# Optimization experiments

Measured on AMD Instinct MI355X. Metric: run time of the kernel, lower is better.

The kernel has to match this reference:

```python
import jax, jax.numpy as jnp
import numpy as np
import math

N_EMBD = 1024
D_STATE = 16
D_CONV = 4
EXPAND = 2
D_INNER = EXPAND * N_EMBD          # 2048
DT_RANK = math.ceil(N_EMBD / 16)   # 64
B, L = 2, 2048
LN_EPS = 1e-5


def setup_inputs() -> dict:
    key = jax.random.key(0)
    ks = jax.random.split(key, 12)
    s = lambda fan_in: 1.0 / np.sqrt(fan_in)
    x = jax.random.normal(ks[0], (B, L, N_EMBD), dtype=jnp.float32)
    ln_g = jnp.ones((N_EMBD,), jnp.float32)
    ln_b = jnp.zeros((N_EMBD,), jnp.float32)
    in_proj_w = jax.random.normal(ks[1], (2 * D_INNER, N_EMBD), jnp.float32) * s(N_EMBD)
    conv_w = jax.random.normal(ks[2], (D_INNER, 1, D_CONV), jnp.float32) * s(D_CONV)
    conv_b = jax.random.normal(ks[3], (D_INNER,), jnp.float32) * s(D_CONV)
    x_proj_w = jax.random.normal(ks[4], (DT_RANK + 2 * D_STATE, D_INNER), jnp.float32) * s(D_INNER)
    dt_proj_w = jax.random.normal(ks[5], (D_INNER, DT_RANK), jnp.float32) * s(DT_RANK)
    # dt bias initialized so softplus(dt) is in a reasonable range
    dt = jnp.exp(jax.random.uniform(ks[6], (D_INNER,)) * (np.log(0.1) - np.log(1e-3)) + np.log(1e-3))
    dt_proj_b = dt + jnp.log(-jnp.expm1(-dt))  # inverse softplus
    A_log = jnp.log(jnp.tile(jnp.arange(1, D_STATE + 1, dtype=jnp.float32)[None, :], (D_INNER, 1)))
    D = jnp.ones((D_INNER,), jnp.float32)
    out_proj_w = jax.random.normal(ks[7], (N_EMBD, D_INNER), jnp.float32) * s(D_INNER)
    return {"x": x, "ln_g": ln_g, "ln_b": ln_b, "in_proj_w": in_proj_w,
            "conv_w": conv_w, "conv_b": conv_b, "x_proj_w": x_proj_w,
            "dt_proj_w": dt_proj_w, "dt_proj_b": dt_proj_b,
            "A_log": A_log, "D": D, "out_proj_w": out_proj_w}


def _selective_scan(u, delta, A, Bt, Ct, D):
    # u, delta: (B, L, d_inner); A: (d_inner, d_state); Bt, Ct: (B, L, d_state)
    def step(h, inp):
        d_t, B_t, C_t, u_t = inp          # (B,di) (B,ds) (B,ds) (B,di)
        dA = jnp.exp(d_t[..., None] * A)                     # (B, di, ds)
        dBu = d_t[..., None] * B_t[:, None, :] * u_t[..., None]
        h = dA * h + dBu
        y = jnp.einsum('bds,bs->bd', h, C_t)
        return h, y
    h0 = jnp.zeros((u.shape[0], A.shape[0], A.shape[1]), u.dtype)
    xs = (jnp.swapaxes(delta, 0, 1), jnp.swapaxes(Bt, 0, 1),
          jnp.swapaxes(Ct, 0, 1), jnp.swapaxes(u, 0, 1))
    _, ys = jax.lax.scan(step, h0, xs)    # (L, B, di)
    return jnp.swapaxes(ys, 0, 1) + u * D


def reference(x, ln_g, ln_b, in_proj_w, conv_w, conv_b, x_proj_w,
              dt_proj_w, dt_proj_b, A_log, D, out_proj_w):
    # Pre-LayerNorm
    mu = jnp.mean(x, axis=-1, keepdims=True)
    var = jnp.var(x, axis=-1, keepdims=True)
    x_norm = (x - mu) * jax.lax.rsqrt(var + LN_EPS) * ln_g + ln_b

    # Input projection -> (u, res)
    xz = jnp.einsum('bld,ed->ble', x_norm, in_proj_w)        # (B, L, 2*di)
    u, res = jnp.split(xz, 2, axis=-1)

    # Causal depthwise conv1d over time
    u_c = jnp.swapaxes(u, 1, 2)                              # (B, di, L)
    u_c = jax.lax.conv_general_dilated(
        u_c, conv_w, window_strides=(1,), padding=[(D_CONV - 1, 0)],
        dimension_numbers=('NCH', 'OIH', 'NCH'), feature_group_count=D_INNER)
    u_c = jax.nn.silu(jnp.swapaxes(u_c, 1, 2) + conv_b)      # (B, L, di)

    # SSM parameterization
    x_dbl = jnp.einsum('bld,ed->ble', u_c, x_proj_w)         # (B, L, dt_rank + 2*ds)
    dt, Bt, Ct = jnp.split(x_dbl, [DT_RANK, DT_RANK + D_STATE], axis=-1)
    delta = jax.nn.softplus(jnp.einsum('blr,dr->bld', dt, dt_proj_w) + dt_proj_b)
    A = -jnp.exp(A_log)                                      # (di, ds)

    y = _selective_scan(u_c, delta, A, Bt, Ct, D)            # (B, L, di)
    y = y * jax.nn.silu(res)
    out = jnp.einsum('bld,ed->ble', y, out_proj_w)           # (B, L, n_embd)
    return x + out
```

## Files before the change

### kernel.cpp

```cpp
#include <hip/hip_runtime.h>
#include <hip/hip_bf16.h>
#include <math.h>

#define NE    1024
#define DI    2048
#define LSEQ  2048
#define NB    2
#define DS    16
#define DTR   64
#define XDW   96

#define CCH   64
#define TCH   (LSEQ/CCH)

#define SKX   8
#define XPROJ_PART (4096*96)

typedef __attribute__((ext_vector_type(8))) short short8;
typedef __attribute__((ext_vector_type(4))) float floatx4;

__device__ __forceinline__ float softplus_fast(float x) {
    return (x > 20.f) ? x : __logf(1.f + __expf(x));
}
__device__ __forceinline__ float siluf(float x) {
    return x / (1.f + __expf(-x));
}

__device__ __forceinline__ void gld16(const void* g, void* l) {
    __builtin_amdgcn_global_load_lds(
        (const __attribute__((address_space(1))) unsigned int*)g,
        (__attribute__((address_space(3))) unsigned int*)l, 16, 0, 0);
}

#define F2BF_N1 (4096*1024/4)
#define F2BF_N2 (2048*1024/4)
#define F2BF_N3 (96*2048/4)
#define F2BF_N4 (2048*64/4)
#define LN_BLOCKS 4096
#define F2BF_BLOCKS ((F2BF_N1 + F2BF_N2 + F2BF_N3 + F2BF_N4) / 256)

__global__ __launch_bounds__(256) void prep_kernel(
    const float* __restrict__ x, const float* __restrict__ g,
    const float* __restrict__ b, __hip_bfloat16* __restrict__ xn,
    const float* __restrict__ s1, ushort4* __restrict__ d1,
    const float* __restrict__ s2, ushort4* __restrict__ d2,
    const float* __restrict__ s3, ushort4* __restrict__ d3,
    const float* __restrict__ s4, ushort4* __restrict__ d4)
{
    int tid = threadIdx.x;
    if (blockIdx.x >= LN_BLOCKS) {
        int i = (blockIdx.x - LN_BLOCKS) * 256 + tid;
        const float* src; ushort4* dst; int j;
        if (i < F2BF_N1)                           { src = s1; dst = d1; j = i; }
        else if (i < F2BF_N1 + F2BF_N2)            { src = s2; dst = d2; j = i - F2BF_N1; }
        else if (i < F2BF_N1 + F2BF_N2 + F2BF_N3)  { src = s3; dst = d3; j = i - F2BF_N1 - F2BF_N2; }
        else                                       { src = s4; dst = d4; j = i - F2BF_N1 - F2BF_N2 - F2BF_N3; }
        float4 v = ((const float4*)src)[j];
        union { __hip_bfloat16 h[4]; ushort4 u; } cv;
        cv.h[0] = __float2bfloat16(v.x);
        cv.h[1] = __float2bfloat16(v.y);
        cv.h[2] = __float2bfloat16(v.z);
        cv.h[3] = __float2bfloat16(v.w);
        dst[j] = cv.u;
        return;
    }
    int row = blockIdx.x;
    const float4* xr = (const float4*)(x + (size_t)row * NE);
    float4 v = xr[tid];
    float s  = v.x + v.y + v.z + v.w;
    float sq = v.x*v.x + v.y*v.y + v.z*v.z + v.w*v.w;
    #pragma unroll
    for (int off = 32; off > 0; off >>= 1) {
        s  += __shfl_down(s, off);
        sq += __shfl_down(sq, off);
    }
    __shared__ float ss[4], ssq[4];
    __shared__ float smu, srstd;
    int wv = tid >> 6, lane = tid & 63;
    if (lane == 0) { ss[wv] = s; ssq[wv] = sq; }
    __syncthreads();
    if (tid == 0) {
        float a = ss[0] + ss[1] + ss[2] + ss[3];
        float q = ssq[0] + ssq[1] + ssq[2] + ssq[3];
        float mu  = a * (1.f / NE);
        float var = q * (1.f / NE) - mu * mu;
        smu = mu; srstd = rsqrtf(var + 1e-5f);
    }
    __syncthreads();
    float mu = smu, rstd = srstd;
    float4 gv = ((const float4*)g)[tid];
    float4 bv = ((const float4*)b)[tid];
    union { __hip_bfloat16 h[4]; ushort4 u; } cv;
    cv.h[0] = __float2bfloat16((v.x - mu) * rstd * gv.x + bv.x);
    cv.h[1] = __float2bfloat16((v.y - mu) * rstd * gv.y + bv.y);
    cv.h[2] = __float2bfloat16((v.z - mu) * rstd * gv.z + bv.z);
    cv.h[3] = __float2bfloat16((v.w - mu) * rstd * gv.w + bv.w);
    ((ushort4*)xn)[row * 256 + tid] = cv.u;
}

__global__ __launch_bounds__(256, 2) void gemm_bf16_in(
    const __hip_bfloat16* __restrict__ A,
    const __hip_bfloat16* __restrict__ W,
    __hip_bfloat16* __restrict__ C, int N, int K)
{
    __shared__ __hip_bfloat16 As[128 * 64];
    __shared__ __hip_bfloat16 Bs[256 * 64];
    int tid = threadIdx.x;
    int lane = tid & 63;
    int w = tid >> 6, wr = w >> 1, wc = w & 1;
    int row0 = blockIdx.y * 128, col0 = blockIdx.x * 256;

    int sr = tid >> 3, sc = tid & 7;
    int gc = sc ^ (sr & 7);
    const __hip_bfloat16* ag = A + (size_t)(row0 + sr) * K + gc * 8;
    const __hip_bfloat16* bg = W + (size_t)(col0 + sr) * K + gc * 8;
    char* la_st = (char*)As + w * 1024;
    char* lb_st = (char*)Bs + w * 1024;
    const size_t rs32 = (size_t)32 * K;

    floatx4 acc[4][8];
    #pragma unroll
    for (int i = 0; i < 4; ++i)
        #pragma unroll
        for (int j = 0; j < 8; ++j) acc[i][j] = (floatx4){0.f, 0.f, 0.f, 0.f};

    int m = lane & 15, kq = lane >> 4;
    int s0 = kq ^ (m & 7);
    int s1 = (4 + kq) ^ (m & 7);
    const char* la0 = (const char*)As + (wr * 64 + m) * 128 + s0 * 16;
    const char* la1 = (const char*)As + (wr * 64 + m) * 128 + s1 * 16;
    const char* lb0 = (const char*)Bs + (wc * 128 + m) * 128 + s0 * 16;
    const char* lb1 = (const char*)Bs + (wc * 128 + m) * 128 + s1 * 16;

    for (int k0 = 0; k0 < K; k0 += 64) {
        #pragma unroll
        for (int j = 0; j < 4; ++j)
            gld16(ag + j * rs32, la_st + j * 4096);
        #pragma unroll
        for (int j = 0; j < 8; ++j)
            gld16(bg + j * rs32, lb_st + j * 4096);
        ag += 64; bg += 64;
        __syncthreads();
        {
            short8 af[4], bf[8];
            #pragma unroll
            for (int i = 0; i < 4; ++i) af[i] = *(const short8*)(la0 + i * 2048);
            #pragma unroll
            for (int j = 0; j < 8; ++j) bf[j] = *(const short8*)(lb0 + j * 2048);
            #pragma unroll
            for (int i = 0; i < 4; ++i)
                #pragma unroll
                for (int j = 0; j < 8; ++j)
                    acc[i][j] = __builtin_amdgcn_mfma_f32_16x16x32_bf16(
                        af[i], bf[j], acc[i][j], 0, 0, 0);
        }
        {
            short8 af[4], bf[8];
            #pragma unroll
            for (int i = 0; i < 4; ++i) af[i] = *(const short8*)(la1 + i * 2048);
            #pragma unroll
            for (int j = 0; j < 8; ++j) bf[j] = *(const short8*)(lb1 + j * 2048);
            #pragma unroll
            for (int i = 0; i < 4; ++i)
                #pragma unroll
                for (int j = 0; j < 8; ++j)
                    acc[i][j] = __builtin_amdgcn_mfma_f32_16x16x32_bf16(
                        af[i], bf[j], acc[i][j], 0, 0, 0);
        }
        __syncthreads();
    }

    int crow = row0 + wr * 64 + kq * 4;
    int ccol = col0 + wc * 128 + m;
    #pragma unroll
    for (int i = 0; i < 4; ++i)
        #pragma unroll
        for (int j = 0; j < 8; ++j)
            #pragma unroll
            for (int r2 = 0; r2 < 4; ++r2) {
                size_t rr = (size_t)(crow + i * 16 + r2);
                int cc = ccol + j * 16;
                C[rr * N + cc] = __float2bfloat16(acc[i][j][r2]);
            }
}

__global__ __launch_bounds__(256) void dtproj_mfma(
    const __hip_bfloat16* __restrict__ A,
    const __hip_bfloat16* __restrict__ W,
    const float* __restrict__ bias,
    __hip_bfloat16* __restrict__ dlt)
{
    __shared__ __hip_bfloat16 As[128 * 64];
    __shared__ __hip_bfloat16 Bs[128 * 64];
    int tid = threadIdx.x;
    int lane = tid & 63;
    int w = tid >> 6, wr = w >> 1, wc = w & 1;
    int row0 = blockIdx.y * 128, col0 = blockIdx.x * 128;
    const int K = DTR;

    int sr = tid >> 3, sc = tid & 7;
    int gc = sc ^ (sr & 7);
    const __hip_bfloat16* ag = A + (size_t)(row0 + sr) * K + gc * 8;
    const __hip_bfloat16* bg = W + (size_t)(col0 + sr) * K + gc * 8;
    char* la_st = (char*)As + w * 1024;
    char* lb_st = (char*)Bs + w * 1024;
    const size_t rs32 = (size_t)32 * K;

    #pragma unroll
    for (int j = 0; j < 4; ++j) {
        gld16(ag + j * rs32, la_st + j * 4096);
        gld16(bg + j * rs32, lb_st + j * 4096);
    }

    floatx4 acc[4][4];
    #pragma unroll
    for (int i = 0; i < 4; ++i)
        #pragma unroll
        for (int j = 0; j < 4; ++j) acc[i][j] = (floatx4){0.f, 0.f, 0.f, 0.f};

    int m = lane & 15, kq = lane >> 4;
    int s0 = kq ^ (m & 7);
    int s1 = (4 + kq) ^ (m & 7);
    const char* la0 = (const char*)As + (wr * 64 + m) * 128 + s0 * 16;
    const char* la1 = (const char*)As + (wr * 64 + m) * 128 + s1 * 16;
    const char* lb0 = (const char*)Bs + (wc * 64 + m) * 128 + s0 * 16;
    const char* lb1 = (const char*)Bs + (wc * 64 + m) * 128 + s1 * 16;
    __syncthreads();
    {
        short8 af[4], bf[4];
        #pragma unroll
        for (int i = 0; i < 4; ++i) {
            af[i] = *(const short8*)(la0 + i * 2048);
            bf[i] = *(const short8*)(lb0 + i * 2048);
        }
        #pragma unroll
        for (int i = 0; i < 4; ++i)
            #pragma unroll
            for (int j = 0; j < 4; ++j)
                acc[i][j] = __builtin_amdgcn_mfma_f32_16x16x32_bf16(
                    af[i], bf[j], acc[i][j], 0, 0, 0);
    }
    {
        short8 af[4], bf[4];
        #pragma unroll
        for (int i = 0; i < 4; ++i) {
            af[i] = *(const short8*)(la1 + i * 2048);
            bf[i] = *(const short8*)(lb1 + i * 2048);
        }
        #pragma unroll
        for (int i = 0; i < 4; ++i)
            #pragma unroll
            for (int j = 0; j < 4; ++j)
                acc[i][j] = __builtin_amdgcn_mfma_f32_16x16x32_bf16(
                    af[i], bf[j], acc[i][j], 0, 0, 0);
    }

    int crow = row0 + wr * 64 + kq * 4;
    int ccol = col0 + wc * 64 + m;
    float bj[4];
    #pragma unroll
    for (int j = 0; j < 4; ++j) bj[j] = bias[ccol + j * 16];
    #pragma unroll
    for (int i = 0; i < 4; ++i)
        #pragma unroll
        for (int j = 0; j < 4; ++j)
            #pragma unroll
            for (int r2 = 0; r2 < 4; ++r2) {
                size_t rr = (size_t)(crow + i * 16 + r2);
                int cc = ccol + j * 16;
                dlt[rr * DI + cc] =
                    __float2bfloat16(softplus_fast(acc[i][j][r2] + bj[j]));
            }
}

__global__ __launch_bounds__(256) void gemm_bf16_n128(
    const __hip_bfloat16* __restrict__ A,
    const __hip_bfloat16* __restrict__ W,
    const float* __restrict__ resid,
    float* __restrict__ C, int N, int K)
{
    __shared__ __hip_bfloat16 As[64 * 64];
    __shared__ __hip_bfloat16 Bs[128 * 64];
    int tid = threadIdx.x;
    int lane = tid & 63;
    int w = tid >> 6;
    int row0 = blockIdx.y * 64, col0 = blockIdx.x * 128;

    int sr = tid >> 3, sc = tid & 7;
    int gc = sc ^ (sr & 7);
    const __hip_bfloat16* ag = A + (size_t)(row0 + sr) * K + gc * 8;
    const __hip_bfloat16* bg = W + (size_t)(col0 + sr) * K + gc * 8;
    char* la_st = (char*)As + w * 1024;
    char* lb_st = (char*)Bs + w * 1024;
    const size_t rs32 = (size_t)32 * K;

    floatx4 acc[4][2];
    #pragma unroll
    for (int i = 0; i < 4; ++i)
        #pragma unroll
        for (int j = 0; j < 2; ++j) acc[i][j] = (floatx4){0.f, 0.f, 0.f, 0.f};

    int m = lane & 15, kq = lane >> 4;
    int s0 = kq ^ (m & 7);
    int s1 = (4 + kq) ^ (m & 7);
    const char* la0 = (const char*)As + m * 128 + s0 * 16;
    const char* la1 = (const char*)As + m * 128 + s1 * 16;
    const char* lb0 = (const char*)Bs + (w * 32 + m) * 128 + s0 * 16;
    const char* lb1 = (const char*)Bs + (w * 32 + m) * 128 + s1 * 16;

    for (int k0 = 0; k0 < K; k0 += 64) {
        gld16(ag,        la_st);
        gld16(ag + rs32, la_st + 4096);
        #pragma unroll
        for (int j = 0; j < 4; ++j)
            gld16(bg + j * rs32, lb_st + j * 4096);
        ag += 64; bg += 64;
        __syncthreads();
        {
            short8 af[4], bf[2];
            #pragma unroll
            for (int i = 0; i < 4; ++i) af[i] = *(const short8*)(la0 + i * 2048);
            #pragma unroll
            for (int j = 0; j < 2; ++j) bf[j] = *(const short8*)(lb0 + j * 2048);
            #pragma unroll
            for (int i = 0; i < 4; ++i)
                #pragma unroll
                for (int j = 0; j < 2; ++j)
                    acc[i][j] = __builtin_amdgcn_mfma_f32_16x16x32_bf16(
                        af[i], bf[j], acc[i][j], 0, 0, 0);
        }
        {
            short8 af[4], bf[2];
            #pragma unroll
            for (int i = 0; i < 4; ++i) af[i] = *(const short8*)(la1 + i * 2048);
            #pragma unroll
            for (int j = 0; j < 2; ++j) bf[j] = *(const short8*)(lb1 + j * 2048);
            #pragma unroll
            for (int i = 0; i < 4; ++i)
                #pragma unroll
                for (int j = 0; j < 2; ++j)
                    acc[i][j] = __builtin_amdgcn_mfma_f32_16x16x32_bf16(
                        af[i], bf[j], acc[i][j], 0, 0, 0);
        }
        __syncthreads();
    }

    int crow = row0 + kq * 4;
    int ccol = col0 + w * 32 + m;
    #pragma unroll
    for (int i = 0; i < 4; ++i)
        #pragma unroll
        for (int j = 0; j < 2; ++j)
            #pragma unroll
            for (int r2 = 0; r2 < 4; ++r2) {
                size_t rr = (size_t)(crow + i * 16 + r2);
                int cc = ccol + j * 16;
                C[rr * N + cc] = acc[i][j][r2] + resid[rr * N + cc];
            }
}

__global__ __launch_bounds__(256) void xproj_kernel(
    const __hip_bfloat16* __restrict__ A,
    const __hip_bfloat16* __restrict__ W,
    float* __restrict__ xpart)
{
    int tid = threadIdx.x;
    int lane = tid & 63;
    int w = tid >> 6;
    int kz = blockIdx.y;
    int row0 = blockIdx.x * 128 + w * 32;
    int m  = lane & 15;
    int kq = lane >> 4;

    floatx4 acc[2][6];
    #pragma unroll
    for (int i = 0; i < 2; ++i)
        #pragma unroll
        for (int j = 0; j < 6; ++j) acc[i][j] = (floatx4){0.f, 0.f, 0.f, 0.f};

    const __hip_bfloat16* a0 = A + (size_t)(row0 + m) * DI + kz * (DI / SKX) + kq * 8;
    const __hip_bfloat16* b0 = W + (size_t)m * DI + kz * (DI / SKX) + kq * 8;

    #pragma unroll
    for (int ks = 0; ks < (DI / SKX) / 32; ++ks) {
        short8 af0 = *(const short8*)(a0);
        short8 af1 = *(const short8*)(a0 + (size_t)16 * DI);
        #pragma unroll
        for (int j = 0; j < 6; ++j) {
            short8 bf = *(const short8*)(b0 + (size_t)j * 16 * DI);
            acc[0][j] = __builtin_amdgcn_mfma_f32_16x16x32_bf16(af0, bf, acc[0][j], 0, 0, 0);
            acc[1][j] = __builtin_amdgcn_mfma_f32_16x16x32_bf16(af1, bf, acc[1][j], 0, 0, 0);
        }
        a0 += 32; b0 += 32;
    }

    float* cp = xpart + (size_t)kz * XPROJ_PART;
    int crow = row0 + kq * 4;
    #pragma unroll
    for (int i = 0; i < 2; ++i)
        #pragma unroll
        for (int j = 0; j < 6; ++j)
            #pragma unroll
            for (int r = 0; r < 4; ++r)
                cp[(size_t)(crow + i * 16 + r) * XDW + j * 16 + m] = acc[i][j][r];
}

__global__ __launch_bounds__(256) void reduce8_kernel(
    const float* __restrict__ part, float* __restrict__ xdbl,
    __hip_bfloat16* __restrict__ dtx)
{
    int i = blockIdx.x * 256 + threadIdx.x;
    float s = 0.f;
    #pragma unroll
    for (int k = 0; k < SKX; ++k) s += part[(size_t)k * XPROJ_PART + i];
    xdbl[i] = s;
    int row = i / XDW;
    int col = i - row * XDW;
    if (col < DTR)
        dtx[(size_t)row * DTR + col] = __float2bfloat16(s);
}

__global__ __launch_bounds__(256) void conv_silu_kernel(
    const __hip_bfloat16* __restrict__ xz, const float* __restrict__ cw,
    const float* __restrict__ cb, ushort4* __restrict__ uc_bf)
{
    int i4 = blockIdx.x * 256 + threadIdx.x;
    int d4 = i4 & 511;
    int bt = i4 >> 9;
    int t  = bt & (LSEQ - 1);
    int d  = d4 * 4;
    float4 w0 = *(const float4*)(cw + (size_t)(d+0) * 4);
    float4 w1 = *(const float4*)(cw + (size_t)(d+1) * 4);
    float4 w2 = *(const float4*)(cw + (size_t)(d+2) * 4);
    float4 w3 = *(const float4*)(cw + (size_t)(d+3) * 4);
    const float* wt0 = (const float*)&w0;
    const float* wt1 = (const float*)&w1;
    const float* wt2 = (const float*)&w2;
    const float* wt3 = (const float*)&w3;
    float4 acc = *(const float4*)(cb + d);
    const __hip_bfloat16* base = xz + ((size_t)bt << 12) + d;
    #pragma unroll
    for (int k = 0; k < 4; ++k) {
        int tp = t - 3 + k;
        if (tp >= 0) {
            union { ushort4 u; __hip_bfloat16 h[4]; } raw;
            raw.u = *(const ushort4*)(base - ((size_t)(3 - k) << 12));
            acc.x = fmaf(wt0[k], __bfloat162float(raw.h[0]), acc.x);
            acc.y = fmaf(wt1[k], __bfloat162float(raw.h[1]), acc.y);
            acc.z = fmaf(wt2[k], __bfloat162float(raw.h[2]), acc.z);
            acc.w = fmaf(wt3[k], __bfloat162float(raw.h[3]), acc.w);
        }
    }
    union { __hip_bfloat16 h[4]; ushort4 u; } cv;
    cv.h[0] = __float2bfloat16(siluf(acc.x));
    cv.h[1] = __float2bfloat16(siluf(acc.y));
    cv.h[2] = __float2bfloat16(siluf(acc.z));
    cv.h[3] = __float2bfloat16(siluf(acc.w));
    uc_bf[i4] = cv.u;
}

template<bool FINAL>
__global__ __launch_bounds__(256) void scan_chunk_kernel(
    const __hip_bfloat16* __restrict__ dlt, const __hip_bfloat16* __restrict__ uc,
    const float* __restrict__ xdbl, const float* __restrict__ A_log,
    const float* __restrict__ Dp, const __hip_bfloat16* __restrict__ xz,
    float* __restrict__ P, float* __restrict__ S,
    __hip_bfloat16* __restrict__ y)
{
    __shared__ float sBC[TCH][32];
    int tid = threadIdx.x;
    int d = blockIdx.x * 256 + tid;
    int c = blockIdx.y;
    int b = blockIdx.z;
    int row0 = b * LSEQ + c * TCH;

    {
        int tt = tid >> 3, j4 = (tid & 7) * 4;
        const float4* src = (const float4*)(xdbl + (size_t)(row0 + tt) * XDW + DTR + j4);
        *(float4*)(&sBC[tt][j4]) = *src;
    }
    __syncthreads();

    float Ac[DS], h[DS], p[DS];
    #pragma unroll
    for (int s = 0; s < DS; ++s) {
        Ac[s] = -expf(A_log[(size_t)d * DS + s]);
        p[s] = 1.f;
    }
    float Ac0 = Ac[0];
    bool fast = true;
    #pragma unroll
    for (int s = 1; s < DS; ++s)
        fast = fast && (fabsf(Ac[s] - (float)(s + 1) * Ac0) <= 1e-3f * fabsf(Ac[s]));

    size_t soff = (((size_t)b * CCH + c) * DI + d) * DS;
    if (FINAL) {
        #pragma unroll
        for (int s = 0; s < DS; ++s) h[s] = S[soff + s];
    } else {
        #pragma unroll
        for (int s = 0; s < DS; ++s) h[s] = 0.f;
    }
    float Dd = Dp[d];
    size_t ix = (size_t)row0 * DI + d;

    if (fast) {
        float p1 = 1.f;
        float dv = __bfloat162float(dlt[ix]);
        float ut = __bfloat162float(uc[ix]);
        for (int tt = 0; tt < TCH; ++tt) {
            float dv_n = 0.f, ut_n = 0.f;
            if (tt + 1 < TCH) {
                dv_n = __bfloat162float(dlt[ix + DI]);
                ut_n = __bfloat162float(uc[ix + DI]);
            }
            float du = dv * ut;
            float e1 = __expf(dv * Ac0);
            float e = 1.f;
            float yacc = 0.f;
            #pragma unroll
            for (int s = 0; s < DS; ++s) {
                e *= e1;
                h[s] = fmaf(e, h[s], du * sBC[tt][s]);
                if (FINAL) yacc = fmaf(h[s], sBC[tt][16 + s], yacc);
            }
            if (!FINAL) p1 *= e1;
            if (FINAL) {
                float res = __bfloat162float(xz[((size_t)(row0 + tt) << 12) + DI + d]);
                y[ix] = __float2bfloat16(fmaf(ut, Dd, yacc) * siluf(res));
            }
            ix += DI;
            dv = dv_n; ut = ut_n;
        }
        if (!FINAL) {
            float e = 1.f;
            #pragma unroll
            for (int s = 0; s < DS; ++s) { e *= p1; p[s] = e; }
        }
    } else {
        for (int tt = 0; tt < TCH; ++tt) {
            float dv = __bfloat162float(dlt[ix]);
            float ut = __bfloat162float(uc[ix]);
            float du = dv * ut;
            float yacc = 0.f;
            #pragma unroll
            for (int s = 0; s < DS; ++s) {
                float e = __expf(dv * Ac[s]);
                h[s] = fmaf(e, h[s], du * sBC[tt][s]);
                if (FINAL) yacc = fmaf(h[s], sBC[tt][16 + s], yacc);
                else       p[s] *= e;
            }
            if (FINAL) {
                float res = __bfloat162float(xz[((size_t)(row0 + tt) << 12) + DI + d]);
                y[ix] = __float2bfloat16(fmaf(ut, Dd, yacc) * siluf(res));
            }
            ix += DI;
        }
    }
    if (!FINAL) {
        #pragma unroll
        for (int s = 0; s < DS; ++s) { P[soff + s] = p[s]; S[soff + s] = h[s]; }
    }
}

__global__ __launch_bounds__(256) void scan_combine_kernel(
    const float* __restrict__ P, float* __restrict__ S)
{
    int idx = blockIdx.x * 256 + threadIdx.x;
    int b = idx >> 15;
    int rest = idx & 32767;
    float h = 0.f;
    for (int c = 0; c < CCH; ++c) {
        size_t off = (((size_t)b * CCH + c) << 15) + rest;
        float tmp = S[off];
        float pv  = P[off];
        S[off] = h;
        h = fmaf(pv, h, tmp);
    }
}

extern "C" void kernel_launch(void* const* d_in, const int* in_sizes, int n_in,
                              void* d_out, int out_size, void* d_ws, size_t ws_size,
                              hipStream_t stream)
{
    const float* x        = (const float*)d_in[0];
    const float* ln_g     = (const float*)d_in[1];
    const float* ln_b     = (const float*)d_in[2];
    const float* in_w     = (const float*)d_in[3];
    const float* conv_w   = (const float*)d_in[4];
    const float* conv_b   = (const float*)d_in[5];
    const float* xproj_w  = (const float*)d_in[6];
    const float* dtproj_w = (const float*)d_in[7];
    const float* dtproj_b = (const float*)d_in[8];
    const float* A_log    = (const float*)d_in[9];
    const float* Dvec     = (const float*)d_in[10];
    const float* out_w    = (const float*)d_in[11];
    float* out = (float*)d_out;

    char* base = (char*)d_ws;
    __hip_bfloat16* xz_bf    = (__hip_bfloat16*)(base + 0);
    __hip_bfloat16* dlt_bf   = (__hip_bfloat16*)(base + 33554432);
    __hip_bfloat16* uc_bf    = (__hip_bfloat16*)(base + 67108864);
    float*          xdbl     = (float*)         (base + 83886080);
    float*          xpart    = (float*)         (base + 85458944);
    float*          Pch      = (float*)         (base + 85458944);
    float*          Sch      = (float*)         (base + 102236160);
    __hip_bfloat16* xnorm_bf = (__hip_bfloat16*)(base + 119013376);
    __hip_bfloat16* yb_bf    = (__hip_bfloat16*)(base + 127401984);
    __hip_bfloat16* inw_bf   = (__hip_bfloat16*)(base + 144179200);
    __hip_bfloat16* outw_bf  = (__hip_bfloat16*)(base + 152567808);
    __hip_bfloat16* xpw_bf   = (__hip_bfloat16*)(base + 156762112);
    __hip_bfloat16* dtx_bf   = (__hip_bfloat16*)(base + 157155328);
    __hip_bfloat16* dtw_bf   = (__hip_bfloat16*)(base + 157679616);

    const int R = NB * LSEQ;

    prep_kernel<<<LN_BLOCKS + F2BF_BLOCKS, 256, 0, stream>>>(
        x, ln_g, ln_b, xnorm_bf,
        in_w, (ushort4*)inw_bf, out_w, (ushort4*)outw_bf,
        xproj_w, (ushort4*)xpw_bf, dtproj_w, (ushort4*)dtw_bf);
    gemm_bf16_in<<<dim3((2*DI)/256, R/128), 256, 0, stream>>>(
        xnorm_bf, inw_bf, xz_bf, 2*DI, NE);
    conv_silu_kernel<<<(R * DI / 4) / 256, 256, 0, stream>>>(
        xz_bf, conv_w, conv_b, (ushort4*)uc_bf);
    xproj_kernel<<<dim3(R/128, SKX), 256, 0, stream>>>(uc_bf, xpw_bf, xpart);
    reduce8_kernel<<<(R * XDW) / 256, 256, 0, stream>>>(xpart, xdbl, dtx_bf);
    dtproj_mfma<<<dim3(DI/128, R/128), 256, 0, stream>>>(
        dtx_bf, dtw_bf, dtproj_b, dlt_bf);
    dim3 gScan(DI / 256, CCH, NB);
    scan_chunk_kernel<false><<<gScan, 256, 0, stream>>>(
        dlt_bf, uc_bf, xdbl, A_log, Dvec, xz_bf, Pch, Sch, yb_bf);
    scan_combine_kernel<<<(NB * DI * DS) / 256, 256, 0, stream>>>(Pch, Sch);
    scan_chunk_kernel<true><<<gScan, 256, 0, stream>>>(
        dlt_bf, uc_bf, xdbl, A_log, Dvec, xz_bf, Pch, Sch, yb_bf);
    gemm_bf16_n128<<<dim3(NE/128, R/64), 256, 0, stream>>>(
        yb_bf, outw_bf, x, out, NE, DI);
}
```

Baseline: 294.2 us.

## Fuse chunked scan passes into single kernel with decoupled look-back

Replaces the three-kernel chunked selective scan (local pass, sequential combine, final pass) with one kernel. Each block publishes its chunk's decay product and local state, then walks back through earlier chunks using flags to get its starting state, and publishes its inclusive state so later chunks can stop early. This removes two launches and the separate combine pass. In exchange it adds atomics, spin-waiting and fences, and it depends on earlier chunks being scheduled first to avoid stalls or deadlock. The state layout is also changed to be coalesced per thread.

Result: slower. 1.128 ms (+283.3%).

```diff
diff --git a/kernel.cpp b/kernel.cpp
--- a/kernel.cpp
+++ b/kernel.cpp
@@ -12,6 +12,7 @@
 
 #define CCH   64
 #define TCH   (LSEQ/CCH)
+#define NREC  (NB*(DI/256)*CCH)
 
 #define SKX   8
 #define XPROJ_PART (4096*96)
@@ -407,9 +408,10 @@
 
 __global__ __launch_bounds__(256) void reduce8_kernel(
     const float* __restrict__ part, float* __restrict__ xdbl,
-    __hip_bfloat16* __restrict__ dtx)
+    __hip_bfloat16* __restrict__ dtx, int* __restrict__ flags)
 {
     int i = blockIdx.x * 256 + threadIdx.x;
+    if (i < NREC) flags[i] = 0;
     float s = 0.f;
     #pragma unroll
     for (int k = 0; k < SKX; ++k) s += part[(size_t)k * XPROJ_PART + i];
@@ -459,20 +461,21 @@
     uc_bf[i4] = cv.u;
 }
 
-template<bool FINAL>
-__global__ __launch_bounds__(256) void scan_chunk_kernel(
+__global__ __launch_bounds__(256, 4) void scan_fused_kernel(
     const __hip_bfloat16* __restrict__ dlt, const __hip_bfloat16* __restrict__ uc,
     const float* __restrict__ xdbl, const float* __restrict__ A_log,
     const float* __restrict__ Dp, const __hip_bfloat16* __restrict__ xz,
-    float* __restrict__ P, float* __restrict__ S,
-    __hip_bfloat16* __restrict__ y)
+    float* __restrict__ pubP, float* __restrict__ pubS, float* __restrict__ pubH,
+    int* __restrict__ flags, __hip_bfloat16* __restrict__ y)
 {
     __shared__ float sBC[TCH][32];
+    __shared__ int sflag;
     int tid = threadIdx.x;
     int d = blockIdx.x * 256 + tid;
     int c = blockIdx.y;
     int b = blockIdx.z;
     int row0 = b * LSEQ + c * TCH;
+    int rec = (b * (DI / 256) + blockIdx.x) * CCH + c;
 
     {
         int tt = tid >> 3, j4 = (tid & 7) * 4;
@@ -486,26 +489,111 @@
     for (int s = 0; s < DS; ++s) {
         Ac[s] = -expf(A_log[(size_t)d * DS + s]);
         p[s] = 1.f;
+        h[s] = 0.f;
     }
     float Ac0 = Ac[0];
     bool fast = true;
     #pragma unroll
     for (int s = 1; s < DS; ++s)
         fast = fast && (fabsf(Ac[s] - (float)(s + 1) * Ac0) <= 1e-3f * fabsf(Ac[s]));
-
-    size_t soff = (((size_t)b * CCH + c) * DI + d) * DS;
-    if (FINAL) {
-        #pragma unroll
-        for (int s = 0; s < DS; ++s) h[s] = S[soff + s];
-    } else {
-        #pragma unroll
-        for (int s = 0; s < DS; ++s) h[s] = 0.f;
-    }
     float Dd = Dp[d];
+
     size_t ix = (size_t)row0 * DI + d;
-
     if (fast) {
         float p1 = 1.f;
+        for (int tt = 0; tt < TCH; ++tt) {
+            float dv = __bfloat162float(dlt[ix]);
+            float ut = __bfloat162float(uc[ix]);
+            float du = dv * ut;
+            float e1 = __expf(dv * Ac0);
+            float e = 1.f;
+            #pragma unroll
+            for (int s = 0; s < DS; ++s) {
+                e *= e1;
+                h[s] = fmaf(e, h[s], du * sBC[tt][s]);
+            }
+            p1 *= e1;
+            ix += DI;
+        }
+        float e = 1.f;
+        #pragma unroll
+        for (int s = 0; s < DS; ++s) { e *= p1; p[s] = e; }
+    } else {
+        for (int tt = 0; tt < TCH; ++tt) {
+            float dv = __bfloat162float(dlt[ix]);
+            float ut = __bfloat162float(uc[ix]);
+            float du = dv * ut;
+            #pragma unroll
+            for (int s = 0; s < DS; ++s) {
+                float e = __expf(dv * Ac[s]);
+                h[s] = fmaf(e, h[s], du * sBC[tt][s]);
+                p[s] *= e;
+            }
+            ix += DI;
+        }
+    }
+
+    size_t pb = (size_t)rec * DS * 256 + tid;
+    #pragma unroll
+    for (int s = 0; s < DS; ++s) {
+        atomicExch(&pubP[pb + (size_t)s * 256], p[s]);
+        atomicExch(&pubS[pb + (size_t)s * 256], h[s]);
+    }
+    __threadfence();
+    __syncthreads();
+    if (tid == 0) atomicExch(&flags[rec], 1);
+
+    float H0[DS];
+    #pragma unroll
+    for (int s = 0; s < DS; ++s) H0[s] = 0.f;
+    if (c > 0) {
+        float prod[DS];
+        #pragma unroll
+        for (int s = 0; s < DS; ++s) prod[s] = 1.f;
+        for (int j = c - 1; j >= 0; --j) {
+            int recj = rec - (c - j);
+            if (tid == 0) {
+                int f = atomicAdd(&flags[recj], 0);
+                while (f == 0) {
+                    __builtin_amdgcn_s_sleep(8);
+                    f = atomicAdd(&flags[recj], 0);
+                }
+                sflag = f;
+            }
+            __syncthreads();
+            int f = sflag;
+            __syncthreads();
+            __threadfence();
+            size_t pj = (size_t)recj * DS * 256 + tid;
+            if (f >= 2) {
+                #pragma unroll
+                for (int s = 0; s < DS; ++s) {
+                    float Hj = atomicAdd(&pubH[pj + (size_t)s * 256], 0.f);
+                    H0[s] = fmaf(prod[s], Hj, H0[s]);
+                }
+                break;
+            }
+            #pragma unroll
+            for (int s = 0; s < DS; ++s) {
+                float Sj = atomicAdd(&pubS[pj + (size_t)s * 256], 0.f);
+                float Pj = atomicAdd(&pubP[pj + (size_t)s * 256], 0.f);
+                H0[s] = fmaf(prod[s], Sj, H0[s]);
+                prod[s] *= Pj;
+            }
+        }
+    }
+
+    #pragma unroll
+    for (int s = 0; s < DS; ++s)
+        atomicExch(&pubH[pb + (size_t)s * 256], fmaf(p[s], H0[s], h[s]));
+    __threadfence();
+    __syncthreads();
+    if (tid == 0) atomicExch(&flags[rec], 2);
+
+    #pragma unroll
+    for (int s = 0; s < DS; ++s) h[s] = H0[s];
+    ix = (size_t)row0 * DI + d;
+    if (fast) {
         float dv = __bfloat162float(dlt[ix]);
         float ut = __bfloat162float(uc[ix]);
         for (int tt = 0; tt < TCH; ++tt) {
@@ -522,20 +610,12 @@
             for (int s = 0; s < DS; ++s) {
                 e *= e1;
                 h[s] = fmaf(e, h[s], du * sBC[tt][s]);
-                if (FINAL) yacc = fmaf(h[s], sBC[tt][16 + s], yacc);
-            }
-            if (!FINAL) p1 *= e1;
-            if (FINAL) {
-                float res = __bfloat162float(xz[((size_t)(row0 + tt) << 12) + DI + d]);
-                y[ix] = __float2bfloat16(fmaf(ut, Dd, yacc) * siluf(res));
-            }
+                yacc = fmaf(h[s], sBC[tt][16 + s], yacc);
+            }
+            float res = __bfloat162float(xz[((size_t)(row0 + tt) << 12) + DI + d]);
+            y[ix] = __float2bfloat16(fmaf(ut, Dd, yacc) * siluf(res));
             ix += DI;
             dv = dv_n; ut = ut_n;
-        }
-        if (!FINAL) {
-            float e = 1.f;
-            #pragma unroll
-            for (int s = 0; s < DS; ++s) { e *= p1; p[s] = e; }
         }
     } else {
         for (int tt = 0; tt < TCH; ++tt) {
@@ -547,35 +627,12 @@
             for (int s = 0; s < DS; ++s) {
                 float e = __expf(dv * Ac[s]);
                 h[s] = fmaf(e, h[s], du * sBC[tt][s]);
-                if (FINAL) yacc = fmaf(h[s], sBC[tt][16 + s], yacc);
-                else       p[s] *= e;
-            }
-            if (FINAL) {
-                float res = __bfloat162float(xz[((size_t)(row0 + tt) << 12) + DI + d]);
-                y[ix] = __float2bfloat16(fmaf(ut, Dd, yacc) * siluf(res));
-            }
+                yacc = fmaf(h[s], sBC[tt][16 + s], yacc);
+            }
+            float res = __bfloat162float(xz[((size_t)(row0 + tt) << 12) + DI + d]);
+            y[ix] = __float2bfloat16(fmaf(ut, Dd, yacc) * siluf(res));
             ix += DI;
         }
-    }
-    if (!FINAL) {
-        #pragma unroll
-        for (int s = 0; s < DS; ++s) { P[soff + s] = p[s]; S[soff + s] = h[s]; }
-    }
-}
-
-__global__ __launch_bounds__(256) void scan_combine_kernel(
-    const float* __restrict__ P, float* __restrict__ S)
-{
-    int idx = blockIdx.x * 256 + threadIdx.x;
-    int b = idx >> 15;
-    int rest = idx & 32767;
-    float h = 0.f;
-    for (int c = 0; c < CCH; ++c) {
-        size_t off = (((size_t)b * CCH + c) << 15) + rest;
-        float tmp = S[off];
-        float pv  = P[off];
-        S[off] = h;
-        h = fmaf(pv, h, tmp);
     }
 }
 
@@ -603,8 +660,8 @@
     __hip_bfloat16* uc_bf    = (__hip_bfloat16*)(base + 67108864);
     float*          xdbl     = (float*)         (base + 83886080);
     float*          xpart    = (float*)         (base + 85458944);
-    float*          Pch      = (float*)         (base + 85458944);
-    float*          Sch      = (float*)         (base + 102236160);
+    float*          pubP     = (float*)         (base + 85458944);
+    float*          pubS     = (float*)         (base + 102236160);
     __hip_bfloat16* xnorm_bf = (__hip_bfloat16*)(base + 119013376);
     __hip_bfloat16* yb_bf    = (__hip_bfloat16*)(base + 127401984);
     __hip_bfloat16* inw_bf   = (__hip_bfloat16*)(base + 144179200);
@@ -612,6 +669,8 @@
     __hip_bfloat16* xpw_bf   = (__hip_bfloat16*)(base + 156762112);
     __hip_bfloat16* dtx_bf   = (__hip_bfloat16*)(base + 157155328);
     __hip_bfloat16* dtw_bf   = (__hip_bfloat16*)(base + 157679616);
+    float*          pubH     = (float*)         (base + 157941760);
+    int*            flags    = (int*)           (base + 174718976);
 
     const int R = NB * LSEQ;
 
@@ -624,15 +683,12 @@
     conv_silu_kernel<<<(R * DI / 4) / 256, 256, 0, stream>>>(
         xz_bf, conv_w, conv_b, (ushort4*)uc_bf);
     xproj_kernel<<<dim3(R/128, SKX), 256, 0, stream>>>(uc_bf, xpw_bf, xpart);
-    reduce8_kernel<<<(R * XDW) / 256, 256, 0, stream>>>(xpart, xdbl, dtx_bf);
+    reduce8_kernel<<<(R * XDW) / 256, 256, 0, stream>>>(xpart, xdbl, dtx_bf, flags);
     dtproj_mfma<<<dim3(DI/128, R/128), 256, 0, stream>>>(
         dtx_bf, dtw_bf, dtproj_b, dlt_bf);
     dim3 gScan(DI / 256, CCH, NB);
-    scan_chunk_kernel<false><<<gScan, 256, 0, stream>>>(
-        dlt_bf, uc_bf, xdbl, A_log, Dvec, xz_bf, Pch, Sch, yb_bf);
-    scan_combine_kernel<<<(NB * DI * DS) / 256, 256, 0, stream>>>(Pch, Sch);
-    scan_chunk_kernel<true><<<gScan, 256, 0, stream>>>(
-        dlt_bf, uc_bf, xdbl, A_log, Dvec, xz_bf, Pch, Sch, yb_bf);
+    scan_fused_kernel<<<gScan, 256, 0, stream>>>(
+        dlt_bf, uc_bf, xdbl, A_log, Dvec, xz_bf, pubP, pubS, pubH, flags, yb_bf);
     gemm_bf16_n128<<<dim3(NE/128, R/64), 256, 0, stream>>>(
         yb_bf, outw_bf, x, out, NE, DI);
 }
```
